# Kernel optimization log

Hardware: AMD Instinct MI355X
Metric: run time of the kernel (lower is better)

## Reference

```python
import jax, jax.numpy as jnp
import numpy as np

WIN_SIZE = 11
WIN_SIGMA = 1.5
DATA_RANGE = 255.0
K1, K2 = 0.01, 0.03


def _gauss_win():
    # matches _fspecial_gauss_1d(11, 1.5)
    coords = jnp.arange(WIN_SIZE, dtype=jnp.float32) - WIN_SIZE // 2
    g = jnp.exp(-(coords ** 2) / (2.0 * WIN_SIGMA ** 2))
    return g / g.sum()


def _gaussian_filter(x, win):
    # separable depthwise blur, 'valid' padding (padding=0 in torch), groups=C
    C = x.shape[1]
    dn = ('NCHW', 'OIHW', 'NCHW')
    kh = jnp.tile(win.reshape(1, 1, WIN_SIZE, 1), (C, 1, 1, 1))
    kw = jnp.tile(win.reshape(1, 1, 1, WIN_SIZE), (C, 1, 1, 1))
    out = jax.lax.conv_general_dilated(x, kh, (1, 1), 'VALID',
                                       dimension_numbers=dn, feature_group_count=C)
    out = jax.lax.conv_general_dilated(out, kw, (1, 1), 'VALID',
                                       dimension_numbers=dn, feature_group_count=C)
    return out


def setup_inputs() -> dict:
    key = jax.random.key(0)
    k1, k2 = jax.random.split(key)
    shape = (16, 3, 512, 512)
    X = jax.random.uniform(k1, shape, dtype=jnp.float32) * DATA_RANGE
    Y = jax.random.uniform(k2, shape, dtype=jnp.float32) * DATA_RANGE
    return {'X': X, 'Y': Y}


def reference(X, Y):
    win = _gauss_win()
    C1 = (K1 * DATA_RANGE) ** 2
    C2 = (K2 * DATA_RANGE) ** 2
    mu1 = _gaussian_filter(X, win)
    mu2 = _gaussian_filter(Y, win)
    mu1_sq = mu1 * mu1
    mu2_sq = mu2 * mu2
    mu1_mu2 = mu1 * mu2
    sigma1_sq = _gaussian_filter(X * X, win) - mu1_sq
    sigma2_sq = _gaussian_filter(Y * Y, win) - mu2_sq
    sigma12 = _gaussian_filter(X * Y, win) - mu1_mu2
    cs_map = (2.0 * sigma12 + C2) / (sigma1_sq + sigma2_sq + C2)
    ssim_map = (2.0 * mu1_mu2 + C1) / (mu1_sq + mu2_sq + C1) * cs_map
    # torch: mean over channel dim then squeeze(0) (no-op for N>1)
    ssim_map = jnp.mean(ssim_map, axis=1)  # [N, H-10, W-10]
    return 1.0 - ssim_map
```

## Files before the change

kernel.cpp:

```cpp
#include <hip/hip_runtime.h>


namespace {

constexpr int NN = 16, CC = 3, HH = 512, WW = 512;
constexpr int OH = HH - 10, OW = WW - 10;
constexpr int TW = 64, TH = 32;
constexpr int HPITCH = 48;
constexpr float C1c = 6.5025f;
constexpr float C2c = 58.5225f;

typedef _Float16 half8   __attribute__((ext_vector_type(8)));
typedef _Float16 half4   __attribute__((ext_vector_type(4)));
typedef float    floatv4 __attribute__((ext_vector_type(4)));

__device__ const float WF[11] = {
    0.00102838f, 0.00759876f, 0.03600077f, 0.10936069f, 0.21300553f,
    0.26601172f,
    0.21300553f, 0.10936069f, 0.03600077f, 0.00759876f, 0.00102838f
};

__device__ inline half8 pack8(const float4& a, const float4& b) {
    half8 h = {(_Float16)a.x, (_Float16)a.y, (_Float16)a.z, (_Float16)a.w,
               (_Float16)b.x, (_Float16)b.y, (_Float16)b.z, (_Float16)b.w};
    return h;
}

__global__ __launch_bounds__(256, 2)
void ssim_kernel(const float* __restrict__ X, const float* __restrict__ Y,
                 float* __restrict__ out)
{
    __shared__ __align__(16) _Float16 s_ht[TW][HPITCH];
    __shared__ _Float16 s_wtab[16];

    const int tid  = threadIdx.x;
    const int lane = tid & 63;
    const int wv   = tid >> 6;
    const int col0 = blockIdx.x * TW;
    const int row0 = blockIdx.y * TH;
    const int n    = blockIdx.z;

    if (tid < 16) s_wtab[tid] = (tid < 11) ? (_Float16)WF[tid] : (_Float16)0.f;
    __syncthreads();

    half8 bfrag;
    {
        const int bn = lane & 15, kq = (lane >> 4) * 8;
        #pragma unroll
        for (int j = 0; j < 8; ++j) {
            int kk = kq + j - bn;
            kk = (kk < 0 || kk > 10) ? 11 : kk;
            bfrag[j] = s_wtab[kk];
        }
    }

    const int arow = lane & 15;
    const int aq   = lane >> 4;
    const int crow = aq * 4;

    int gcol = col0 + wv * 16 + aq * 8;
    gcol = gcol <= WW - 8 ? gcol : WW - 8;
    int grow[3];
    #pragma unroll
    for (int rc = 0; rc < 3; ++rc) {
        int g = row0 + rc * 16 + arow;
        grow[rc] = g < HH ? g : HH - 1;
    }

    float acc[2][4] = {{0.f,0.f,0.f,0.f},{0.f,0.f,0.f,0.f}};

    const size_t plane = (size_t)HH * WW;
    const float* Xn = X + (size_t)n * CC * plane;
    const float* Yn = Y + (size_t)n * CC * plane;
    const floatv4 zf = {0.f, 0.f, 0.f, 0.f};

    for (int ch = 0; ch < CC; ++ch) {
        const float* Xc = Xn + (size_t)ch * plane;
        const float* Yc = Yn + (size_t)ch * plane;

        float4 fx[3][2], fy[3][2];
        #pragma unroll
        for (int rc = 0; rc < 3; ++rc) {
            const float* bx = Xc + (size_t)grow[rc] * WW + gcol;
            const float* by = Yc + (size_t)grow[rc] * WW + gcol;
            fx[rc][0] = *(const float4*)bx;
            fx[rc][1] = *(const float4*)(bx + 4);
            fy[rc][0] = *(const float4*)by;
            fy[rc][1] = *(const float4*)(by + 4);
        }

        half8 axf[3], ayf[3];
        #pragma unroll
        for (int rc = 0; rc < 3; ++rc) {
            axf[rc] = pack8(fx[rc][0], fx[rc][1]);
            ayf[rc] = pack8(fy[rc][0], fy[rc][1]);
        }

        floatv4 vfr[5][2];
        #pragma unroll
        for (int q = 0; q < 5; ++q) {
            #pragma unroll
            for (int rc = 0; rc < 3; ++rc) {
                half8 a;
                if      (q == 0) a = axf[rc];
                else if (q == 1) a = ayf[rc];
                else if (q == 2) a = axf[rc] * axf[rc];
                else if (q == 3) a = ayf[rc] * ayf[rc];
                else             a = axf[rc] * ayf[rc];
                floatv4 d = __builtin_amdgcn_mfma_f32_16x16x32_f16(
                    a, bfrag, zf, 0, 0, 0);
                half4 h = {(_Float16)d[0], (_Float16)d[1],
                           (_Float16)d[2], (_Float16)d[3]};
                *(half4*)&s_ht[wv*16 + arow][rc*16 + crow] = h;
            }
            #pragma unroll
            for (int b = 0; b < 2; ++b) {
                half8 av = *(const half8*)&s_ht[wv*16 + arow][b*16 + aq*8];
                vfr[q][b] = __builtin_amdgcn_mfma_f32_16x16x32_f16(
                    av, bfrag, zf, 0, 0, 0);
            }
        }

        #pragma unroll
        for (int b = 0; b < 2; ++b) {
            #pragma unroll
            for (int p = 0; p < 4; ++p) {
                float m1 = vfr[0][b][p], m2 = vfr[1][b][p];
                float exx = vfr[2][b][p], eyy = vfr[3][b][p],
                      exy = vfr[4][b][p];
                float m1s = m1*m1, m2s = m2*m2, m12 = m1*m2;
                float s1 = exx - m1s, s2 = eyy - m2s, s12 = exy - m12;
                float n1 = 2.f*m12 + C1c, d1 = m1s + m2s + C1c;
                float n2 = 2.f*s12 + C2c, d2 = s1 + s2 + C2c;
                acc[b][p] = fmaf(n1 * n2, __builtin_amdgcn_rcpf(d1 * d2),
                                 acc[b][p]);
            }
        }
    }

    #pragma unroll
    for (int b = 0; b < 2; ++b) {
        const int orow = row0 + b*16 + arow;
        const int ocol = col0 + wv*16 + crow;
        if (orow < OH) {
            float r0v = 1.f - acc[b][0] * (1.f/3.f);
            float r1v = 1.f - acc[b][1] * (1.f/3.f);
            float r2v = 1.f - acc[b][2] * (1.f/3.f);
            float r3v = 1.f - acc[b][3] * (1.f/3.f);
            size_t base = ((size_t)n * OH + orow) * OW + ocol;
            if (ocol + 3 < OW) {
                *(float2*)(out + base)     = make_float2(r0v, r1v);
                *(float2*)(out + base + 2) = make_float2(r2v, r3v);
            } else {
                float rs[4] = {r0v, r1v, r2v, r3v};
                #pragma unroll
                for (int p = 0; p < 4; ++p)
                    if (ocol + p < OW) out[base + p] = rs[p];
            }
        }
    }
}

}

extern "C" void kernel_launch(void* const* d_in, const int* in_sizes, int n_in,
                              void* d_out, int out_size, void* d_ws, size_t ws_size,
                              hipStream_t stream) {
    const float* X = (const float*)d_in[0];
    const float* Y = (const float*)d_in[1];
    float* out = (float*)d_out;

    dim3 grid((OW + TW - 1) / TW,
              (OH + TH - 1) / TH,
              NN);
    ssim_kernel<<<grid, 256, 0, stream>>>(X, Y, out);
}
```

Before: 141.8 us.

## Split channels across waves and reduce SSIM via shared memory

Each block now uses six waves, two column chunks times three channels, so each wave handles one channel instead of looping over all three. Channel partial SSIM values are summed through a shared-memory buffer after a barrier. Global loads are issued before the weight-fragment setup to expose more memory parallelism, and the horizontal-pass scratch is double-buffered per wave. The tile width is halved, which doubles the block count and the halo overhead, and the shared-memory reduction and barrier add a cost.

Result: slower. 148.9 us (+5.0%).

```diff
diff --git a/kernel.cpp b/kernel.cpp
--- a/kernel.cpp
+++ b/kernel.cpp
@@ -5,8 +5,8 @@
 
 constexpr int NN = 16, CC = 3, HH = 512, WW = 512;
 constexpr int OH = HH - 10, OW = WW - 10;
-constexpr int TW = 64, TH = 32;
-constexpr int HPITCH = 48;
+constexpr int TWB = 32, TH = 32;
+constexpr int HP = 56;
 constexpr float C1c = 6.5025f;
 constexpr float C2c = 58.5225f;
 
@@ -26,26 +26,58 @@
     return h;
 }
 
-__global__ __launch_bounds__(256, 2)
+__global__ __launch_bounds__(384, 8)
 void ssim_kernel(const float* __restrict__ X, const float* __restrict__ Y,
                  float* __restrict__ out)
 {
-    __shared__ __align__(16) _Float16 s_ht[TW][HPITCH];
+    __shared__ __align__(16) _Float16 s_ht[6][2][16][HP];
+    __shared__ __align__(16) float    s_red[2][2][64][8];
     __shared__ _Float16 s_wtab[16];
 
-    const int tid  = threadIdx.x;
-    const int lane = tid & 63;
-    const int wv   = tid >> 6;
-    const int col0 = blockIdx.x * TW;
-    const int row0 = blockIdx.y * TH;
-    const int n    = blockIdx.z;
+    const int tid   = threadIdx.x;
+    const int lane  = tid & 63;
+    const int wv    = tid >> 6;
+    const int chunk = wv / 3;
+    const int ch    = wv % 3;
+    const int col0  = blockIdx.x * TWB;
+    const int row0  = blockIdx.y * TH;
+    const int n     = blockIdx.z;
 
     if (tid < 16) s_wtab[tid] = (tid < 11) ? (_Float16)WF[tid] : (_Float16)0.f;
     __syncthreads();
 
+    const int arow = lane & 15;
+    const int aq   = lane >> 4;
+    const int crow = aq * 4;
+
+    int gcol = col0 + chunk * 16 + aq * 8;
+    gcol = gcol <= WW - 8 ? gcol : WW - 8;
+    int voff[3];
+    #pragma unroll
+    for (int rc = 0; rc < 3; ++rc) {
+        int g = row0 + rc * 16 + arow;
+        g = g < HH ? g : HH - 1;
+        voff[rc] = g * WW + gcol;
+    }
+
+    const size_t plane = (size_t)HH * WW;
+    const float* Xc = X + ((size_t)n * CC + ch) * plane;
+    const float* Yc = Y + ((size_t)n * CC + ch) * plane;
+
+    float4 fx[3][2], fy[3][2];
+    #pragma unroll
+    for (int rc = 0; rc < 3; ++rc) {
+        const float* bx = Xc + voff[rc];
+        const float* by = Yc + voff[rc];
+        fx[rc][0] = *(const float4*)bx;
+        fx[rc][1] = *(const float4*)(bx + 4);
+        fy[rc][0] = *(const float4*)by;
+        fy[rc][1] = *(const float4*)(by + 4);
+    }
+
     half8 bfrag;
     {
-        const int bn = lane & 15, kq = (lane >> 4) * 8;
+        const int bn = lane & 15, kq = aq * 8;
         #pragma unroll
         for (int j = 0; j < 8; ++j) {
             int kk = kq + j - bn;
@@ -54,108 +86,93 @@
         }
     }
 
-    const int arow = lane & 15;
-    const int aq   = lane >> 4;
-    const int crow = aq * 4;
-
-    int gcol = col0 + wv * 16 + aq * 8;
-    gcol = gcol <= WW - 8 ? gcol : WW - 8;
-    int grow[3];
+    half8 axf[3], ayf[3];
     #pragma unroll
     for (int rc = 0; rc < 3; ++rc) {
-        int g = row0 + rc * 16 + arow;
-        grow[rc] = g < HH ? g : HH - 1;
+        axf[rc] = pack8(fx[rc][0], fx[rc][1]);
+        ayf[rc] = pack8(fy[rc][0], fy[rc][1]);
     }
 
-    float acc[2][4] = {{0.f,0.f,0.f,0.f},{0.f,0.f,0.f,0.f}};
-
-    const size_t plane = (size_t)HH * WW;
-    const float* Xn = X + (size_t)n * CC * plane;
-    const float* Yn = Y + (size_t)n * CC * plane;
     const floatv4 zf = {0.f, 0.f, 0.f, 0.f};
 
-    for (int ch = 0; ch < CC; ++ch) {
-        const float* Xc = Xn + (size_t)ch * plane;
-        const float* Yc = Yn + (size_t)ch * plane;
-
-        float4 fx[3][2], fy[3][2];
+    floatv4 vfr[5][2];
+    #pragma unroll
+    for (int qi = 0; qi < 5; ++qi) {
         #pragma unroll
         for (int rc = 0; rc < 3; ++rc) {
-            const float* bx = Xc + (size_t)grow[rc] * WW + gcol;
-            const float* by = Yc + (size_t)grow[rc] * WW + gcol;
-            fx[rc][0] = *(const float4*)bx;
-            fx[rc][1] = *(const float4*)(bx + 4);
-            fy[rc][0] = *(const float4*)by;
-            fy[rc][1] = *(const float4*)(by + 4);
+            half8 a;
+            if      (qi == 0) a = axf[rc] * ayf[rc];
+            else if (qi == 1) a = axf[rc] * axf[rc];
+            else if (qi == 2) a = axf[rc];
+            else if (qi == 3) a = ayf[rc] * ayf[rc];
+            else              a = ayf[rc];
+            floatv4 d = __builtin_amdgcn_mfma_f32_16x16x32_f16(
+                a, bfrag, zf, 0, 0, 0);
+            half4 h = {(_Float16)d[0], (_Float16)d[1],
+                       (_Float16)d[2], (_Float16)d[3]};
+            *(half4*)&s_ht[wv][qi & 1][arow][rc * 16 + crow] = h;
         }
-
-        half8 axf[3], ayf[3];
-        #pragma unroll
-        for (int rc = 0; rc < 3; ++rc) {
-            axf[rc] = pack8(fx[rc][0], fx[rc][1]);
-            ayf[rc] = pack8(fy[rc][0], fy[rc][1]);
-        }
-
-        floatv4 vfr[5][2];
-        #pragma unroll
-        for (int q = 0; q < 5; ++q) {
-            #pragma unroll
-            for (int rc = 0; rc < 3; ++rc) {
-                half8 a;
-                if      (q == 0) a = axf[rc];
-                else if (q == 1) a = ayf[rc];
-                else if (q == 2) a = axf[rc] * axf[rc];
-                else if (q == 3) a = ayf[rc] * ayf[rc];
-                else             a = axf[rc] * ayf[rc];
-                floatv4 d = __builtin_amdgcn_mfma_f32_16x16x32_f16(
-                    a, bfrag, zf, 0, 0, 0);
-                half4 h = {(_Float16)d[0], (_Float16)d[1],
-                           (_Float16)d[2], (_Float16)d[3]};
-                *(half4*)&s_ht[wv*16 + arow][rc*16 + crow] = h;
-            }
-            #pragma unroll
-            for (int b = 0; b < 2; ++b) {
-                half8 av = *(const half8*)&s_ht[wv*16 + arow][b*16 + aq*8];
-                vfr[q][b] = __builtin_amdgcn_mfma_f32_16x16x32_f16(
-                    av, bfrag, zf, 0, 0, 0);
-            }
-        }
-
         #pragma unroll
         for (int b = 0; b < 2; ++b) {
-            #pragma unroll
-            for (int p = 0; p < 4; ++p) {
-                float m1 = vfr[0][b][p], m2 = vfr[1][b][p];
-                float exx = vfr[2][b][p], eyy = vfr[3][b][p],
-                      exy = vfr[4][b][p];
-                float m1s = m1*m1, m2s = m2*m2, m12 = m1*m2;
-                float s1 = exx - m1s, s2 = eyy - m2s, s12 = exy - m12;
-                float n1 = 2.f*m12 + C1c, d1 = m1s + m2s + C1c;
-                float n2 = 2.f*s12 + C2c, d2 = s1 + s2 + C2c;
-                acc[b][p] = fmaf(n1 * n2, __builtin_amdgcn_rcpf(d1 * d2),
-                                 acc[b][p]);
-            }
+            half8 av = *(const half8*)&s_ht[wv][qi & 1][arow][b * 16 + aq * 8];
+            vfr[qi][b] = __builtin_amdgcn_mfma_f32_16x16x32_f16(
+                av, bfrag, zf, 0, 0, 0);
         }
     }
 
+    float res[2][4];
     #pragma unroll
     for (int b = 0; b < 2; ++b) {
-        const int orow = row0 + b*16 + arow;
-        const int ocol = col0 + wv*16 + crow;
-        if (orow < OH) {
-            float r0v = 1.f - acc[b][0] * (1.f/3.f);
-            float r1v = 1.f - acc[b][1] * (1.f/3.f);
-            float r2v = 1.f - acc[b][2] * (1.f/3.f);
-            float r3v = 1.f - acc[b][3] * (1.f/3.f);
-            size_t base = ((size_t)n * OH + orow) * OW + ocol;
-            if (ocol + 3 < OW) {
-                *(float2*)(out + base)     = make_float2(r0v, r1v);
-                *(float2*)(out + base + 2) = make_float2(r2v, r3v);
-            } else {
-                float rs[4] = {r0v, r1v, r2v, r3v};
-                #pragma unroll
-                for (int p = 0; p < 4; ++p)
-                    if (ocol + p < OW) out[base + p] = rs[p];
+        #pragma unroll
+        for (int p = 0; p < 4; ++p) {
+            float m1 = vfr[2][b][p], m2 = vfr[4][b][p];
+            float exx = vfr[1][b][p], eyy = vfr[3][b][p],
+                  exy = vfr[0][b][p];
+            float m1s = m1*m1, m2s = m2*m2, m12 = m1*m2;
+            float s1 = exx - m1s, s2 = eyy - m2s, s12 = exy - m12;
+            float n1 = 2.f*m12 + C1c, d1 = m1s + m2s + C1c;
+            float n2 = 2.f*s12 + C2c, d2 = s1 + s2 + C2c;
+            res[b][p] = fmaf(n1 * n2, __builtin_amdgcn_rcpf(d1 * d2), 0.f);
+        }
+    }
+
+    if (ch != 0) {
+        *(float4*)&s_red[chunk][ch - 1][lane][0] =
+            make_float4(res[0][0], res[0][1], res[0][2], res[0][3]);
+        *(float4*)&s_red[chunk][ch - 1][lane][4] =
+            make_float4(res[1][0], res[1][1], res[1][2], res[1][3]);
+    }
+    __syncthreads();
+
+    if (ch == 0) {
+        #pragma unroll
+        for (int cc = 0; cc < 2; ++cc) {
+            float4 r0 = *(const float4*)&s_red[chunk][cc][lane][0];
+            float4 r1 = *(const float4*)&s_red[chunk][cc][lane][4];
+            res[0][0] += r0.x; res[0][1] += r0.y;
+            res[0][2] += r0.z; res[0][3] += r0.w;
+            res[1][0] += r1.x; res[1][1] += r1.y;
+            res[1][2] += r1.z; res[1][3] += r1.w;
+        }
+        #pragma unroll
+        for (int b = 0; b < 2; ++b) {
+            const int orow = row0 + b * 16 + arow;
+            const int ocol = col0 + chunk * 16 + crow;
+            if (orow < OH) {
+                float r0v = 1.f - res[b][0] * (1.f/3.f);
+                float r1v = 1.f - res[b][1] * (1.f/3.f);
+                float r2v = 1.f - res[b][2] * (1.f/3.f);
+                float r3v = 1.f - res[b][3] * (1.f/3.f);
+                size_t base = ((size_t)n * OH + orow) * OW + ocol;
+                if (ocol + 3 < OW) {
+                    *(float2*)(out + base)     = make_float2(r0v, r1v);
+                    *(float2*)(out + base + 2) = make_float2(r2v, r3v);
+                } else {
+                    float rs[4] = {r0v, r1v, r2v, r3v};
+                    #pragma unroll
+                    for (int p = 0; p < 4; ++p)
+                        if (ocol + p < OW) out[base + p] = rs[p];
+                }
             }
         }
     }
@@ -170,8 +187,8 @@
     const float* Y = (const float*)d_in[1];
     float* out = (float*)d_out;
 
-    dim3 grid((OW + TW - 1) / TW,
-              (OH + TH - 1) / TH,
+    dim3 grid((OW + TWB - 1) / TWB,
+              (OH + TH  - 1) / TH,
               NN);
-    ssim_kernel<<<grid, 256, 0, stream>>>(X, Y, out);
+    ssim_kernel<<<grid, 384, 0, stream>>>(X, Y, out);
 }
```
